# Kernel optimization log

Hardware: AMD Instinct MI355X
Metric: run time of the kernel (lower is better)

The kernel has to match this reference:

```python
import jax, jax.numpy as jnp
import numpy as np

H = W = 56; WS = 7; SHIFT = 3; NH = 6; DIM = 192; DEPTH = 2
HD = DIM // NH; NW = (H // WS) * (W // WS); N = WS * WS; SCALE = HD ** -0.5

# relative position index (constant, as in WindowAttention.__init__)
_c = np.stack(np.meshgrid(np.arange(WS), np.arange(WS), indexing='ij')).reshape(2, -1)
_r = (_c[:, :, None] - _c[:, None, :]).transpose(1, 2, 0)
_r[..., 0] += WS - 1; _r[..., 1] += WS - 1; _r[..., 0] *= 2 * WS - 1
RPI = jnp.asarray(_r.sum(-1).reshape(-1))  # (N*N,)

def _build_mask():
    # shifted-window attention mask (constant, built in SwinTransformerBlock.__init__)
    img = np.zeros((H, W))
    sl = (slice(0, -WS), slice(-WS, -SHIFT), slice(-SHIFT, None))
    cnt = 0
    for hs in sl:
        for ws_ in sl:
            img[hs, ws_] = cnt; cnt += 1
    mw = img.reshape(H // WS, WS, W // WS, WS).transpose(0, 2, 1, 3).reshape(-1, N)
    am = mw[:, None, :] - mw[:, :, None]  # (nW, N, N)
    return jnp.asarray(np.where(am != 0, -100.0, 0.0).astype(np.float32))

MASK = _build_mask()

def _ln(x, g, b):
    m = jnp.mean(x, -1, keepdims=True)
    v = jnp.mean((x - m) ** 2, -1, keepdims=True)
    return (x - m) * jax.lax.rsqrt(v + 1e-5) * g + b

def setup_inputs() -> dict:
    key = jax.random.key(0)
    ks = jax.random.split(key, 8)
    B = 64; s = 0.02
    return {
        'x': jax.random.normal(ks[0], (B, H * W, DIM), jnp.float32),
        'norm1_g': jnp.ones((DEPTH, DIM), jnp.float32),
        'norm1_b': jnp.zeros((DEPTH, DIM), jnp.float32),
        'qkv_w': jax.random.normal(ks[1], (DEPTH, DIM, 3 * DIM), jnp.float32) * s,
        'qkv_b': jnp.zeros((DEPTH, 3 * DIM), jnp.float32),
        'rpb': jax.random.normal(ks[2], (DEPTH, (2 * WS - 1) ** 2, NH), jnp.float32) * s,
        'proj_w': jax.random.normal(ks[3], (DEPTH, DIM, DIM), jnp.float32) * s,
        'proj_b': jnp.zeros((DEPTH, DIM), jnp.float32),
        'norm2_g': jnp.ones((DEPTH, DIM), jnp.float32),
        'norm2_b': jnp.zeros((DEPTH, DIM), jnp.float32),
        'fc1_w': jax.random.normal(ks[4], (DEPTH, DIM, 4 * DIM), jnp.float32) * s,
        'fc1_b': jnp.zeros((DEPTH, 4 * DIM), jnp.float32),
        'fc2_w': jax.random.normal(ks[5], (DEPTH, 4 * DIM, DIM), jnp.float32) * s,
        'fc2_b': jnp.zeros((DEPTH, DIM), jnp.float32),
    }

def reference(x, norm1_g, norm1_b, qkv_w, qkv_b, rpb, proj_w, proj_b,
              norm2_g, norm2_b, fc1_w, fc1_b, fc2_w, fc2_b):
    B = x.shape[0]
    for i in range(DEPTH):
        shift = 0 if i % 2 == 0 else WS // 2
        # --- windowed MHSA branch ---
        h = _ln(x, norm1_g[i], norm1_b[i]).reshape(B, H, W, DIM)
        if shift:
            h = jnp.roll(h, (-shift, -shift), (1, 2))
        # window partition -> (B*nW, N, C)
        w = h.reshape(B, H // WS, WS, W // WS, WS, DIM)
        w = w.transpose(0, 1, 3, 2, 4, 5).reshape(B * NW, N, DIM)
        qkv = (w @ qkv_w[i] + qkv_b[i]).reshape(B * NW, N, 3, NH, HD)
        qkv = qkv.transpose(2, 0, 3, 1, 4)  # (3, Bw, NH, N, HD)
        q, k, v = qkv[0] * SCALE, qkv[1], qkv[2]
        attn = jnp.einsum('bhnd,bhmd->bhnm', q, k)  # (Bw, NH, N, N)
        bias = rpb[i][RPI].reshape(N, N, NH).transpose(2, 0, 1)
        attn = attn + bias[None]
        if shift:
            attn = attn.reshape(B, NW, NH, N, N) + MASK[None, :, None]
            attn = attn.reshape(B * NW, NH, N, N)
        attn = jax.nn.softmax(attn, axis=-1)
        o = jnp.einsum('bhnm,bhmd->bhnd', attn, v)
        o = o.transpose(0, 2, 1, 3).reshape(B * NW, N, DIM)
        o = o @ proj_w[i] + proj_b[i]
        # window reverse
        h = o.reshape(B, H // WS, W // WS, WS, WS, DIM)
        h = h.transpose(0, 1, 3, 2, 4, 5).reshape(B, H, W, DIM)
        if shift:
            h = jnp.roll(h, (shift, shift), (1, 2))
        x = x + h.reshape(B, H * W, DIM)
        # --- MLP branch ---
        m = _ln(x, norm2_g[i], norm2_b[i])
        m = jax.nn.gelu(m @ fc1_w[i] + fc1_b[i], approximate=False)
        x = x + (m @ fc2_w[i] + fc2_b[i])
    return x
```

## Files before the change

### kernel.cpp

```cpp
#include <hip/hip_runtime.h>
#include <stdint.h>

#define NTOK   49
#define DIMC   192
#define NHEAD  6
#define HDIM   32
#define BATCH  64
#define MROWS  (BATCH * 64 * NTOK)
#define SCALE_ 0.17677669529663687f

typedef __attribute__((ext_vector_type(8))) short bf16x8;
typedef __attribute__((ext_vector_type(4))) float f32x4;

union V8 { uint4 u; unsigned short s[8]; };

__device__ __forceinline__ float bf2f(unsigned short u) {
  union { unsigned int i; float f; } c; c.i = ((unsigned int)u) << 16; return c.f;
}
__device__ __forceinline__ unsigned short f2bf(float f) {
  union { float f; unsigned int i; } c; c.f = f;
  unsigned int lsb = (c.i >> 16) & 1;
  return (unsigned short)((c.i + 0x7fffu + lsb) >> 16);
}

template<bool WINDOWED>
__global__ __launch_bounds__(256) void ln_k(const float* __restrict__ X,
    const float* __restrict__ g, const float* __restrict__ b,
    unsigned short* __restrict__ out, int shift)
{
  int wr = blockIdx.x * 4 + (threadIdx.x >> 6);
  int lane = threadIdx.x & 63;
  size_t srow;
  if (WINDOWED) {
    int win = wr / 49, n = wr % 49;
    int bi = win >> 6, w64 = win & 63;
    int wh = w64 >> 3, ww = w64 & 7;
    int ti = n / 7, tj = n % 7;
    int gh = wh * 7 + ti + shift; if (gh >= 56) gh -= 56;
    int gw = ww * 7 + tj + shift; if (gw >= 56) gw -= 56;
    srow = (size_t)bi * 3136 + gh * 56 + gw;
  } else {
    srow = (size_t)wr;
  }
  const float* xr = X + srow * 192;
  float v0 = xr[lane], v1 = xr[lane + 64], v2 = xr[lane + 128];
  float s  = v0 + v1 + v2;
  float s2 = v0*v0 + v1*v1 + v2*v2;
  #pragma unroll
  for (int m = 32; m >= 1; m >>= 1) { s += __shfl_xor(s, m); s2 += __shfl_xor(s2, m); }
  float mean = s * (1.0f/192.0f);
  float var  = s2 * (1.0f/192.0f) - mean*mean;
  float inv  = rsqrtf(var + 1e-5f);
  unsigned short* orow = out + (size_t)wr * 192;
  orow[lane]       = f2bf((v0-mean)*inv*g[lane]      + b[lane]);
  orow[lane+64]    = f2bf((v1-mean)*inv*g[lane+64]   + b[lane+64]);
  orow[lane+128]   = f2bf((v2-mean)*inv*g[lane+128]  + b[lane+128]);
}

template<int EPI, int K>
__global__ __launch_bounds__(256) void gemm_k(
    const unsigned short* __restrict__ A,
    const float* __restrict__ W,
    const float* __restrict__ bias,
    unsigned short* __restrict__ Cbf,
    const float* __restrict__ Xres,
    float* __restrict__ Xdst,
    int N, int shift)
{
  __shared__ unsigned short As[128][40];
  __shared__ unsigned short Bs[64][40];
  const int tid = threadIdx.x;
  const int lane = tid & 63, wv = tid >> 6;
  const int wm = wv >> 1, wn = wv & 1;
  const int row0 = blockIdx.x * 128;
  const int n0   = blockIdx.y * 64;
  f32x4 acc[4][2] = {};
  const int sr  = tid >> 1, ssg = (tid & 1) * 16;
  const int bk  = tid >> 3, bsg = (tid & 7) * 8;
  for (int k0 = 0; k0 < K; k0 += 32) {
    const uint4* asrc = reinterpret_cast<const uint4*>(A + (size_t)(row0 + sr) * K + k0 + ssg);
    uint4 av0 = asrc[0], av1 = asrc[1];
    const float4* wsrc = reinterpret_cast<const float4*>(W + (size_t)(k0 + bk) * N + n0 + bsg);
    float4 w0 = wsrc[0], w1 = wsrc[1];
    __syncthreads();
    *reinterpret_cast<uint4*>(&As[sr][ssg])     = av0;
    *reinterpret_cast<uint4*>(&As[sr][ssg + 8]) = av1;
    Bs[bsg+0][bk] = f2bf(w0.x); Bs[bsg+1][bk] = f2bf(w0.y);
    Bs[bsg+2][bk] = f2bf(w0.z); Bs[bsg+3][bk] = f2bf(w0.w);
    Bs[bsg+4][bk] = f2bf(w1.x); Bs[bsg+5][bk] = f2bf(w1.y);
    Bs[bsg+6][bk] = f2bf(w1.z); Bs[bsg+7][bk] = f2bf(w1.w);
    __syncthreads();
    const int fr = lane & 15, kq = (lane >> 4) * 8;
    bf16x8 bfr[2];
    #pragma unroll
    for (int ni = 0; ni < 2; ++ni)
      bfr[ni] = *reinterpret_cast<const bf16x8*>(&Bs[wn*32 + ni*16 + fr][kq]);
    #pragma unroll
    for (int mi = 0; mi < 4; ++mi) {
      bf16x8 afr = *reinterpret_cast<const bf16x8*>(&As[wm*64 + mi*16 + fr][kq]);
      #pragma unroll
      for (int ni = 0; ni < 2; ++ni)
        acc[mi][ni] = __builtin_amdgcn_mfma_f32_16x16x32_bf16(afr, bfr[ni], acc[mi][ni], 0, 0, 0);
    }
  }
  const int lcol = lane & 15, lr4 = (lane >> 4) * 4;
  #pragma unroll
  for (int mi = 0; mi < 4; ++mi)
  #pragma unroll
  for (int ni = 0; ni < 2; ++ni)
  #pragma unroll
  for (int i = 0; i < 4; ++i) {
    int gr = row0 + wm*64 + mi*16 + lr4 + i;
    int gc = n0 + wn*32 + ni*16 + lcol;
    float v = acc[mi][ni][i] + bias[gc];
    if (EPI == 0) {
      Cbf[(size_t)gr * N + gc] = f2bf(v);
    } else if (EPI == 2) {
      float gv = 0.5f * v * (1.0f + erff(v * 0.70710678118654752f));
      Cbf[(size_t)gr * N + gc] = f2bf(gv);
    } else if (EPI == 1) {
      int win = gr / 49, n = gr % 49;
      int bi = win >> 6, w64 = win & 63;
      int wh = w64 >> 3, ww = w64 & 7;
      int ti = n / 7, tj = n % 7;
      int gh = wh*7 + ti + shift; if (gh >= 56) gh -= 56;
      int gw = ww*7 + tj + shift; if (gw >= 56) gw -= 56;
      size_t idx = ((size_t)bi * 3136 + gh * 56 + gw) * 192 + gc;
      Xdst[idx] = Xres[idx] + v;
    } else {
      size_t idx = (size_t)gr * 192 + gc;
      Xdst[idx] = Xres[idx] + v;
    }
  }
}

template<bool SHIFTED>
__global__ __launch_bounds__(64) void attn_k(
    const unsigned short* __restrict__ qkv,
    const float* __restrict__ rpb,
    unsigned short* __restrict__ out)
{
  __shared__ float kv[2][49][32];
  int blk = blockIdx.x;
  int win = blk / 6, h = blk - win * 6;
  int lane = threadIdx.x;
  const unsigned short* base = qkv + (size_t)win * 49 * 576;
  for (int idx = lane; idx < 196; idx += 64) {
    int n = idx >> 2, sg = (idx & 3) * 8;
    V8 kk, vv;
    kk.u = *reinterpret_cast<const uint4*>(base + n*576 + 192 + h*32 + sg);
    vv.u = *reinterpret_cast<const uint4*>(base + n*576 + 384 + h*32 + sg);
    #pragma unroll
    for (int j = 0; j < 8; ++j) { kv[0][n][sg+j] = bf2f(kk.s[j]); kv[1][n][sg+j] = bf2f(vv.s[j]); }
  }
  __syncthreads();
  if (lane < 49) {
    float q[32];
    const unsigned short* qr = base + (size_t)lane * 576 + h * 32;
    #pragma unroll
    for (int sg = 0; sg < 4; ++sg) {
      V8 qq; qq.u = *reinterpret_cast<const uint4*>(qr + sg*8);
      #pragma unroll
      for (int j = 0; j < 8; ++j) q[sg*8+j] = bf2f(qq.s[j]) * SCALE_;
    }
    int ti = lane / 7, tj = lane - ti * 7;
    int wi = win & 63, wh = wi >> 3, ww = wi & 7;
    int rid = 0;
    if (SHIFTED) {
      int hh = wh*7 + ti, wg = ww*7 + tj;
      rid = (hh < 49 ? 0 : (hh < 53 ? 1 : 2)) * 3 + (wg < 49 ? 0 : (wg < 53 ? 1 : 2));
    }
    float s[49];
    float mx = -1e30f;
    #pragma unroll
    for (int m = 0; m < 49; ++m) {
      float a = 0.f;
      #pragma unroll
      for (int d4 = 0; d4 < 8; ++d4) {
        float4 kf = *reinterpret_cast<const float4*>(&kv[0][m][d4*4]);
        a += q[d4*4+0]*kf.x + q[d4*4+1]*kf.y + q[d4*4+2]*kf.z + q[d4*4+3]*kf.w;
      }
      int mi = m / 7, mj = m - mi * 7;
      a += rpb[((ti - mi + 6) * 13 + (tj - mj + 6)) * 6 + h];
      if (SHIFTED) {
        int hh = wh*7 + mi, wg = ww*7 + mj;
        int rid2 = (hh < 49 ? 0 : (hh < 53 ? 1 : 2)) * 3 + (wg < 49 ? 0 : (wg < 53 ? 1 : 2));
        if (rid2 != rid) a -= 100.f;
      }
      s[m] = a;
      mx = fmaxf(mx, a);
    }
    float sum = 0.f;
    #pragma unroll
    for (int m = 0; m < 49; ++m) { float e = __expf(s[m] - mx); s[m] = e; sum += e; }
    float rs = 1.f / sum;
    float o[32];
    #pragma unroll
    for (int d = 0; d < 32; ++d) o[d] = 0.f;
    #pragma unroll
    for (int m = 0; m < 49; ++m) {
      float p = s[m] * rs;
      #pragma unroll
      for (int d4 = 0; d4 < 8; ++d4) {
        float4 vf = *reinterpret_cast<const float4*>(&kv[1][m][d4*4]);
        o[d4*4+0] += p*vf.x; o[d4*4+1] += p*vf.y; o[d4*4+2] += p*vf.z; o[d4*4+3] += p*vf.w;
      }
    }
    unsigned short* orow = out + ((size_t)win * 49 + lane) * 192 + h * 32;
    #pragma unroll
    for (int sg = 0; sg < 4; ++sg) {
      V8 pk;
      #pragma unroll
      for (int j = 0; j < 8; ++j) pk.s[j] = f2bf(o[sg*8+j]);
      *reinterpret_cast<uint4*>(orow + sg*8) = pk.u;
    }
  }
}

extern "C" void kernel_launch(void* const* d_in, const int* in_sizes, int n_in,
                              void* d_out, int out_size, void* d_ws, size_t ws_size,
                              hipStream_t stream) {
  const float* x    = (const float*)d_in[0];
  const float* n1g  = (const float*)d_in[1];
  const float* n1b  = (const float*)d_in[2];
  const float* qkvw = (const float*)d_in[3];
  const float* qkvb = (const float*)d_in[4];
  const float* rpb  = (const float*)d_in[5];
  const float* pw   = (const float*)d_in[6];
  const float* pb   = (const float*)d_in[7];
  const float* n2g  = (const float*)d_in[8];
  const float* n2b  = (const float*)d_in[9];
  const float* f1w  = (const float*)d_in[10];
  const float* f1b  = (const float*)d_in[11];
  const float* f2w  = (const float*)d_in[12];
  const float* f2b  = (const float*)d_in[13];
  float* out = (float*)d_out;

  const size_t XBYTES = (size_t)MROWS * 192 * 4;
  const size_t ABYTES = (size_t)MROWS * 192 * 2;
  char* ws = (char*)d_ws;
  float* x1 = (float*)ws;
  unsigned short* Abuf = (unsigned short*)(ws + XBYTES);
  unsigned short* Bbuf = (unsigned short*)(ws + XBYTES + ABYTES);

  const int LNBLK = MROWS / 4;
  const dim3 G_QKV(MROWS/128, 9), G_P(MROWS/128, 3), G_F1(MROWS/128, 12), G_F2(MROWS/128, 3);

  for (int i = 0; i < 2; ++i) {
    int shift = i ? 3 : 0;
    const float* xin = i ? (const float*)x1 : x;
    float* xfin = i ? out : x1;
    ln_k<true><<<LNBLK, 256, 0, stream>>>(xin, n1g + i*192, n1b + i*192, Abuf, shift);
    gemm_k<0,192><<<G_QKV, 256, 0, stream>>>(Abuf, qkvw + (size_t)i*192*576, qkvb + i*576,
                                             Bbuf, nullptr, nullptr, 576, 0);
    if (shift) attn_k<true ><<<BATCH*64*NHEAD, 64, 0, stream>>>(Bbuf, rpb + i*169*6, Abuf);
    else       attn_k<false><<<BATCH*64*NHEAD, 64, 0, stream>>>(Bbuf, rpb + i*169*6, Abuf);
    gemm_k<1,192><<<G_P, 256, 0, stream>>>(Abuf, pw + (size_t)i*192*192, pb + i*192,
                                           nullptr, xin, x1, 192, shift);
    ln_k<false><<<LNBLK, 256, 0, stream>>>(x1, n2g + i*192, n2b + i*192, Abuf, 0);
    gemm_k<2,192><<<G_F1, 256, 0, stream>>>(Abuf, f1w + (size_t)i*192*768, f1b + i*768,
                                            Bbuf, nullptr, nullptr, 768, 0);
    gemm_k<3,768><<<G_F2, 256, 0, stream>>>(Bbuf, f2w + (size_t)i*768*192, f2b + i*192,
                                            nullptr, x1, xfin, 192, 0);
  }
}
```

Measured before the change: 2.113 ms.

## Fuse LN2+FC1+GELU+FC2 into one MLP kernel and pre-transpose weights to bf16

Adds a kernel that converts and transposes all weights to bf16 once per call. GEMMs now read B fragments directly from global or L2 instead of staging them through LDS with per-element conversion. Replaces the LN2, FC1 and FC2 launches with one fused kernel that keeps a 64-row tile's normalized input and hidden activations in shared memory, so the 768-wide hidden tensor never goes to HBM. This cuts global traffic and launch count, at the cost of large LDS use, lower occupancy and uncoalesced weight fragment loads.

```diff
diff --git a/kernel.cpp b/kernel.cpp
--- a/kernel.cpp
+++ b/kernel.cpp
@@ -2,9 +2,6 @@
 #include <stdint.h>
 
 #define NTOK   49
-#define DIMC   192
-#define NHEAD  6
-#define HDIM   32
 #define BATCH  64
 #define MROWS  (BATCH * 64 * NTOK)
 #define SCALE_ 0.17677669529663687f
@@ -23,25 +20,29 @@
   return (unsigned short)((c.i + 0x7fffu + lsb) >> 16);
 }
 
-template<bool WINDOWED>
+__global__ __launch_bounds__(256) void wt_k(const float* __restrict__ W,
+    unsigned short* __restrict__ Wt, int K, int N)
+{
+  int idx = blockIdx.x * 256 + threadIdx.x;
+  if (idx < K * N) {
+    int k = idx / N, n = idx - k * N;
+    Wt[(size_t)n * K + k] = f2bf(W[idx]);
+  }
+}
+
 __global__ __launch_bounds__(256) void ln_k(const float* __restrict__ X,
     const float* __restrict__ g, const float* __restrict__ b,
     unsigned short* __restrict__ out, int shift)
 {
   int wr = blockIdx.x * 4 + (threadIdx.x >> 6);
   int lane = threadIdx.x & 63;
-  size_t srow;
-  if (WINDOWED) {
-    int win = wr / 49, n = wr % 49;
-    int bi = win >> 6, w64 = win & 63;
-    int wh = w64 >> 3, ww = w64 & 7;
-    int ti = n / 7, tj = n % 7;
-    int gh = wh * 7 + ti + shift; if (gh >= 56) gh -= 56;
-    int gw = ww * 7 + tj + shift; if (gw >= 56) gw -= 56;
-    srow = (size_t)bi * 3136 + gh * 56 + gw;
-  } else {
-    srow = (size_t)wr;
-  }
+  int win = wr / 49, n = wr % 49;
+  int bi = win >> 6, w64 = win & 63;
+  int wh = w64 >> 3, ww = w64 & 7;
+  int ti = n / 7, tj = n % 7;
+  int gh = wh * 7 + ti + shift; if (gh >= 56) gh -= 56;
+  int gw = ww * 7 + tj + shift; if (gw >= 56) gw -= 56;
+  size_t srow = (size_t)bi * 3136 + gh * 56 + gw;
   const float* xr = X + srow * 192;
   float v0 = xr[lane], v1 = xr[lane + 64], v2 = xr[lane + 128];
   float s  = v0 + v1 + v2;
@@ -57,10 +58,10 @@
   orow[lane+128]   = f2bf((v2-mean)*inv*g[lane+128]  + b[lane+128]);
 }
 
-template<int EPI, int K>
-__global__ __launch_bounds__(256) void gemm_k(
+template<int EPI>
+__global__ __launch_bounds__(256) void gemm2_k(
     const unsigned short* __restrict__ A,
-    const float* __restrict__ W,
+    const unsigned short* __restrict__ Wt,
     const float* __restrict__ bias,
     unsigned short* __restrict__ Cbf,
     const float* __restrict__ Xres,
@@ -68,7 +69,6 @@
     int N, int shift)
 {
   __shared__ unsigned short As[128][40];
-  __shared__ unsigned short Bs[64][40];
   const int tid = threadIdx.x;
   const int lane = tid & 63, wv = tid >> 6;
   const int wm = wv >> 1, wn = wv & 1;
@@ -76,25 +76,19 @@
   const int n0   = blockIdx.y * 64;
   f32x4 acc[4][2] = {};
   const int sr  = tid >> 1, ssg = (tid & 1) * 16;
-  const int bk  = tid >> 3, bsg = (tid & 7) * 8;
-  for (int k0 = 0; k0 < K; k0 += 32) {
-    const uint4* asrc = reinterpret_cast<const uint4*>(A + (size_t)(row0 + sr) * K + k0 + ssg);
+  const int fr = lane & 15, kq = (lane >> 4) * 8;
+  #pragma unroll
+  for (int k0 = 0; k0 < 192; k0 += 32) {
+    const uint4* asrc = reinterpret_cast<const uint4*>(A + (size_t)(row0 + sr) * 192 + k0 + ssg);
     uint4 av0 = asrc[0], av1 = asrc[1];
-    const float4* wsrc = reinterpret_cast<const float4*>(W + (size_t)(k0 + bk) * N + n0 + bsg);
-    float4 w0 = wsrc[0], w1 = wsrc[1];
     __syncthreads();
     *reinterpret_cast<uint4*>(&As[sr][ssg])     = av0;
     *reinterpret_cast<uint4*>(&As[sr][ssg + 8]) = av1;
-    Bs[bsg+0][bk] = f2bf(w0.x); Bs[bsg+1][bk] = f2bf(w0.y);
-    Bs[bsg+2][bk] = f2bf(w0.z); Bs[bsg+3][bk] = f2bf(w0.w);
-    Bs[bsg+4][bk] = f2bf(w1.x); Bs[bsg+5][bk] = f2bf(w1.y);
-    Bs[bsg+6][bk] = f2bf(w1.z); Bs[bsg+7][bk] = f2bf(w1.w);
     __syncthreads();
-    const int fr = lane & 15, kq = (lane >> 4) * 8;
     bf16x8 bfr[2];
     #pragma unroll
     for (int ni = 0; ni < 2; ++ni)
-      bfr[ni] = *reinterpret_cast<const bf16x8*>(&Bs[wn*32 + ni*16 + fr][kq]);
+      bfr[ni] = *reinterpret_cast<const bf16x8*>(&Wt[(size_t)(n0 + wn*32 + ni*16 + fr) * 192 + k0 + kq]);
     #pragma unroll
     for (int mi = 0; mi < 4; ++mi) {
       bf16x8 afr = *reinterpret_cast<const bf16x8*>(&As[wm*64 + mi*16 + fr][kq]);
@@ -115,10 +109,7 @@
     float v = acc[mi][ni][i] + bias[gc];
     if (EPI == 0) {
       Cbf[(size_t)gr * N + gc] = f2bf(v);
-    } else if (EPI == 2) {
-      float gv = 0.5f * v * (1.0f + erff(v * 0.70710678118654752f));
-      Cbf[(size_t)gr * N + gc] = f2bf(gv);
-    } else if (EPI == 1) {
+    } else {
       int win = gr / 49, n = gr % 49;
       int bi = win >> 6, w64 = win & 63;
       int wh = w64 >> 3, ww = w64 & 7;
@@ -127,10 +118,101 @@
       int gw = ww*7 + tj + shift; if (gw >= 56) gw -= 56;
       size_t idx = ((size_t)bi * 3136 + gh * 56 + gw) * 192 + gc;
       Xdst[idx] = Xres[idx] + v;
-    } else {
-      size_t idx = (size_t)gr * 192 + gc;
-      Xdst[idx] = Xres[idx] + v;
-    }
+    }
+  }
+}
+
+__global__ __launch_bounds__(512, 4) void mlp_k(
+    const float* __restrict__ X,
+    const float* __restrict__ g, const float* __restrict__ b,
+    const unsigned short* __restrict__ W1t,
+    const float* __restrict__ b1,
+    const unsigned short* __restrict__ W2t,
+    const float* __restrict__ b2,
+    float* __restrict__ Y)
+{
+  __shared__ unsigned short As[64][200];
+  __shared__ unsigned short Hs[64][396];
+  const int row0 = blockIdx.x * 64;
+  const int tid = threadIdx.x, lane = tid & 63, wv = tid >> 6;
+  #pragma unroll
+  for (int r = 0; r < 8; ++r) {
+    int row = wv * 8 + r;
+    const float* xr = X + (size_t)(row0 + row) * 192;
+    float v0 = xr[lane], v1 = xr[lane + 64], v2 = xr[lane + 128];
+    float s  = v0 + v1 + v2;
+    float s2 = v0*v0 + v1*v1 + v2*v2;
+    #pragma unroll
+    for (int m = 32; m >= 1; m >>= 1) { s += __shfl_xor(s, m); s2 += __shfl_xor(s2, m); }
+    float mean = s * (1.0f/192.0f);
+    float var  = s2 * (1.0f/192.0f) - mean*mean;
+    float inv  = rsqrtf(var + 1e-5f);
+    As[row][lane]       = f2bf((v0-mean)*inv*g[lane]      + b[lane]);
+    As[row][lane+64]    = f2bf((v1-mean)*inv*g[lane+64]   + b[lane+64]);
+    As[row][lane+128]   = f2bf((v2-mean)*inv*g[lane+128]  + b[lane+128]);
+  }
+  __syncthreads();
+  const int fr = lane & 15, kq = (lane >> 4) * 8;
+  const int lcol = lane & 15, lr4 = (lane >> 4) * 4;
+  const int wm2 = wv >> 2, wn2 = wv & 3;
+  f32x4 acc2[2][3] = {};
+  for (int hh = 0; hh < 2; ++hh) {
+    f32x4 acc1[4][3] = {};
+    const int c0 = hh * 384 + wv * 48;
+    #pragma unroll
+    for (int k0 = 0; k0 < 192; k0 += 32) {
+      bf16x8 bfr[3];
+      #pragma unroll
+      for (int ni = 0; ni < 3; ++ni)
+        bfr[ni] = *reinterpret_cast<const bf16x8*>(&W1t[(size_t)(c0 + ni*16 + fr) * 192 + k0 + kq]);
+      #pragma unroll
+      for (int mi = 0; mi < 4; ++mi) {
+        bf16x8 afr = *reinterpret_cast<const bf16x8*>(&As[mi*16 + fr][k0 + kq]);
+        #pragma unroll
+        for (int ni = 0; ni < 3; ++ni)
+          acc1[mi][ni] = __builtin_amdgcn_mfma_f32_16x16x32_bf16(afr, bfr[ni], acc1[mi][ni], 0, 0, 0);
+      }
+    }
+    #pragma unroll
+    for (int mi = 0; mi < 4; ++mi)
+    #pragma unroll
+    for (int ni = 0; ni < 3; ++ni)
+    #pragma unroll
+    for (int i = 0; i < 4; ++i) {
+      int rr = mi*16 + lr4 + i;
+      int cc = wv*48 + ni*16 + lcol;
+      float v = acc1[mi][ni][i] + b1[hh*384 + cc];
+      float gv = 0.5f * v * (1.0f + erff(v * 0.70710678118654752f));
+      Hs[rr][cc] = f2bf(gv);
+    }
+    __syncthreads();
+    #pragma unroll
+    for (int k0 = 0; k0 < 384; k0 += 32) {
+      bf16x8 bfr[3];
+      #pragma unroll
+      for (int ni = 0; ni < 3; ++ni)
+        bfr[ni] = *reinterpret_cast<const bf16x8*>(&W2t[(size_t)(wn2*48 + ni*16 + fr) * 768 + hh*384 + k0 + kq]);
+      #pragma unroll
+      for (int mi = 0; mi < 2; ++mi) {
+        bf16x8 afr = *reinterpret_cast<const bf16x8*>(&Hs[wm2*32 + mi*16 + fr][k0 + kq]);
+        #pragma unroll
+        for (int ni = 0; ni < 3; ++ni)
+          acc2[mi][ni] = __builtin_amdgcn_mfma_f32_16x16x32_bf16(afr, bfr[ni], acc2[mi][ni], 0, 0, 0);
+      }
+    }
+    __syncthreads();
+  }
+  #pragma unroll
+  for (int mi = 0; mi < 2; ++mi)
+  #pragma unroll
+  for (int ni = 0; ni < 3; ++ni)
+  #pragma unroll
+  for (int i = 0; i < 4; ++i) {
+    int grow = row0 + wm2*32 + mi*16 + lr4 + i;
+    int gc = wn2*48 + ni*16 + lcol;
+    float v = acc2[mi][ni][i] + b2[gc];
+    size_t idx = (size_t)grow * 192 + gc;
+    Y[idx] = X[idx] + v;
   }
 }
 
@@ -238,29 +320,38 @@
 
   const size_t XBYTES = (size_t)MROWS * 192 * 4;
   const size_t ABYTES = (size_t)MROWS * 192 * 2;
+  const size_t QBYTES = (size_t)MROWS * 576 * 2;
   char* ws = (char*)d_ws;
   float* x1 = (float*)ws;
   unsigned short* Abuf = (unsigned short*)(ws + XBYTES);
   unsigned short* Bbuf = (unsigned short*)(ws + XBYTES + ABYTES);
+  unsigned short* WT   = (unsigned short*)(ws + XBYTES + ABYTES + QBYTES);
+  const size_t WQ = 110592, WP = 36864, W1 = 147456, W2 = 147456;
+  const size_t WD = WQ + WP + W1 + W2;
+
+  for (int d = 0; d < 2; ++d) {
+    unsigned short* wt = WT + d * WD;
+    wt_k<<<(int)((WQ + 255)/256), 256, 0, stream>>>(qkvw + (size_t)d*WQ, wt,                 192, 576);
+    wt_k<<<(int)((WP + 255)/256), 256, 0, stream>>>(pw   + (size_t)d*WP, wt + WQ,            192, 192);
+    wt_k<<<(int)((W1 + 255)/256), 256, 0, stream>>>(f1w  + (size_t)d*W1, wt + WQ + WP,       192, 768);
+    wt_k<<<(int)((W2 + 255)/256), 256, 0, stream>>>(f2w  + (size_t)d*W2, wt + WQ + WP + W1,  768, 192);
+  }
 
   const int LNBLK = MROWS / 4;
-  const dim3 G_QKV(MROWS/128, 9), G_P(MROWS/128, 3), G_F1(MROWS/128, 12), G_F2(MROWS/128, 3);
+  const dim3 G_QKV(MROWS/128, 9), G_P(MROWS/128, 3);
 
   for (int i = 0; i < 2; ++i) {
     int shift = i ? 3 : 0;
     const float* xin = i ? (const float*)x1 : x;
     float* xfin = i ? out : x1;
-    ln_k<true><<<LNBLK, 256, 0, stream>>>(xin, n1g + i*192, n1b + i*192, Abuf, shift);
-    gemm_k<0,192><<<G_QKV, 256, 0, stream>>>(Abuf, qkvw + (size_t)i*192*576, qkvb + i*576,
-                                             Bbuf, nullptr, nullptr, 576, 0);
-    if (shift) attn_k<true ><<<BATCH*64*NHEAD, 64, 0, stream>>>(Bbuf, rpb + i*169*6, Abuf);
-    else       attn_k<false><<<BATCH*64*NHEAD, 64, 0, stream>>>(Bbuf, rpb + i*169*6, Abuf);
-    gemm_k<1,192><<<G_P, 256, 0, stream>>>(Abuf, pw + (size_t)i*192*192, pb + i*192,
-                                           nullptr, xin, x1, 192, shift);
-    ln_k<false><<<LNBLK, 256, 0, stream>>>(x1, n2g + i*192, n2b + i*192, Abuf, 0);
-    gemm_k<2,192><<<G_F1, 256, 0, stream>>>(Abuf, f1w + (size_t)i*192*768, f1b + i*768,
-                                            Bbuf, nullptr, nullptr, 768, 0);
-    gemm_k<3,768><<<G_F2, 256, 0, stream>>>(Bbuf, f2w + (size_t)i*768*192, f2b + i*192,
-                                            nullptr, x1, xfin, 192, 0);
-  }
-}
+    const unsigned short* wt = WT + i * WD;
+    ln_k<<<LNBLK, 256, 0, stream>>>(xin, n1g + i*192, n1b + i*192, Abuf, shift);
+    gemm2_k<0><<<G_QKV, 256, 0, stream>>>(Abuf, wt, qkvb + i*576, Bbuf, nullptr, nullptr, 576, 0);
+    if (shift) attn_k<true ><<<BATCH*64*6, 64, 0, stream>>>(Bbuf, rpb + i*169*6, Abuf);
+    else       attn_k<false><<<BATCH*64*6, 64, 0, stream>>>(Bbuf, rpb + i*169*6, Abuf);
+    gemm2_k<1><<<G_P, 256, 0, stream>>>(Abuf, wt + WQ, pb + i*192, nullptr, xin, x1, 192, shift);
+    mlp_k<<<MROWS/64, 512, 0, stream>>>(x1, n2g + i*192, n2b + i*192,
+                                        wt + WQ + WP, f1b + i*768,
+                                        wt + WQ + WP + W1, f2b + i*192, xfin);
+  }
+}
```

After: 1.882 ms. -10.9%, faster.
